# Kernel optimization log

Hardware: AMD Instinct MI355X
Metric: run time of the kernel (lower is better)

## Reference

```python
import jax, jax.numpy as jnp
import numpy as np
import math

B, N, H, C = 1, 2048, 8, 128
PQ, PV, R, CS, CZ = 8, 12, 2, 256, 128
CZ4 = CZ // 4
INF = 1e5
EPS = 1e-8
SOFTPLUS_INV_1 = 0.541324854612918


def _quat_to_rot(q):
    q = q / jnp.linalg.norm(q, axis=-1, keepdims=True)
    w, x, y, z = q[..., 0], q[..., 1], q[..., 2], q[..., 3]
    return jnp.stack([
        jnp.stack([1 - 2 * (y * y + z * z), 2 * (x * y - z * w), 2 * (x * z + y * w)], -1),
        jnp.stack([2 * (x * y + z * w), 1 - 2 * (x * x + z * z), 2 * (y * z - x * w)], -1),
        jnp.stack([2 * (x * z - y * w), 2 * (y * z + x * w), 1 - 2 * (x * x + y * y)], -1),
    ], -2)


def setup_inputs() -> dict:
    key = jax.random.key(0)
    ks = jax.random.split(key, 16)
    rn = lambda k, shape, s=1.0: jax.random.normal(k, shape, dtype=jnp.float32) * s
    hc = H * C
    return dict(
        s=rn(ks[0], (B, N, CS)),
        z_factor_1=rn(ks[1], (B, N, R, CZ)),
        z_factor_2=rn(ks[2], (B, N, R, CZ)),
        rot=_quat_to_rot(rn(ks[3], (B, N, 4))),
        trans=rn(ks[4], (B, N, 3)),
        mask=jnp.ones((B, N), dtype=bool),
        w_q=rn(ks[5], (hc, CS), 0.02), b_q=jnp.zeros((hc,), jnp.float32),
        w_kv=rn(ks[6], (2 * hc, CS), 0.02), b_kv=jnp.zeros((2 * hc,), jnp.float32),
        w_qp=rn(ks[7], (H * PQ * 3, CS), 0.02), b_qp=jnp.zeros((H * PQ * 3,), jnp.float32),
        w_kvp=rn(ks[8], (H * (PQ + PV) * 3, CS), 0.02), b_kvp=jnp.zeros((H * (PQ + PV) * 3,), jnp.float32),
        w_b=rn(ks[9], (H, CZ), 0.02), b_b=jnp.zeros((H,), jnp.float32),
        w_dz=rn(ks[10], (CZ4, CZ), 0.02), b_dz=jnp.zeros((CZ4,), jnp.float32),
        head_weights=jnp.full((H,), SOFTPLUS_INV_1, dtype=jnp.float32),
        w_out=rn(ks[11], (CS, H * (CZ4 + C + 4 * PV)), 0.02), b_out=jnp.zeros((CS,), jnp.float32),
    )


def _lin(x, w, b):
    return x @ w.T + b


def _ipa(s, z1, z2, rot, trans, mask, w_q, b_q, w_kv, b_kv, w_qp, b_qp,
         w_kvp, b_kvp, w_b, b_b, w_dz, b_dz, head_weights, w_out, b_out):
    q = _lin(s, w_q, b_q).reshape(B, N, H, C)
    kv = _lin(s, w_kv, b_kv).reshape(B, N, H, 2 * C)
    k, v = kv[..., :C], kv[..., C:]
    # local points -> global frame: x_glob = R x_loc + t
    qp = _lin(s, w_qp, b_qp).reshape(B, N, H * PQ, 3)
    qp = (jnp.einsum('bnij,bnpj->bnpi', rot, qp) + trans[:, :, None, :]).reshape(B, N, H, PQ, 3)
    kvp = _lin(s, w_kvp, b_kvp).reshape(B, N, H * (PQ + PV), 3)
    kvp = (jnp.einsum('bnij,bnpj->bnpi', rot, kvp) + trans[:, :, None, :]).reshape(B, N, H, PQ + PV, 3)
    kp, vp = kvp[..., :PQ, :], kvp[..., PQ:, :]
    # head weights: softplus init to 1, AF2 scaling sqrt(1/(3*(PQ*9/2)))
    hw = jax.nn.softplus(head_weights) * math.sqrt(1.0 / (3 * (PQ * 9.0 / 2)))
    # low-rank pair bias factors
    b1 = _lin(z1, w_b, b_b)   # [B,N,R,H]
    b2 = _lin(z2, w_b, b_b)
    z1d = _lin(z1, w_dz, b_dz)  # [B,N,R,CZ4]
    z2d = _lin(z2, w_dz, b_dz)
    # logits: scalar QK + point-distance + low-rank pair bias
    scalar = jnp.einsum('bihc,bjhc->bhij', q, k) * math.sqrt(1.0 / (3 * C))
    ptdot = jnp.einsum('bihpx,bjhpx->bhij', qp, kp)
    qn = jnp.sum(qp * qp, axis=(-1, -2))  # [B,N,H]
    kn = jnp.sum(kp * kp, axis=(-1, -2))
    pt_term = hw[None, :, None, None] * (
        ptdot - 0.5 * qn.transpose(0, 2, 1)[:, :, :, None] - 0.5 * kn.transpose(0, 2, 1)[:, :, None, :])
    pair = jnp.einsum('birh,bjrh->bhij', b1, b2)
    mask_bias = jnp.where(mask, 0.0, -INF)[:, None, None, :]
    a = jax.nn.softmax(scalar + pt_term + pair + mask_bias, axis=-1)  # [B,H,N,N]
    # outputs
    o = jnp.einsum('bhij,bjhc->bihc', a, v).reshape(B, N, H * C)
    opt = jnp.einsum('bhij,bjhpx->bihpx', a, vp)  # global-frame points
    opt_loc = jnp.einsum('bnji,bnhpj->bnhpi', rot, opt - trans[:, :, None, None, :])  # R^T (x - t)
    opt_norm = jnp.sqrt(jnp.sum(opt_loc * opt_loc, axis=-1) + EPS)  # [B,N,H,PV]
    oz = jnp.einsum('bhij,bjrc->bihrc', a, z2d)
    opair = jnp.sum(oz * z1d[:, :, None, :, :], axis=3)  # [B,N,H,CZ4]
    feats = jnp.concatenate([
        o,
        opt_loc[..., 0].reshape(B, N, H * PV),
        opt_loc[..., 1].reshape(B, N, H * PV),
        opt_loc[..., 2].reshape(B, N, H * PV),
        opt_norm.reshape(B, N, H * PV),
        opair.reshape(B, N, H * CZ4),
    ], axis=-1)
    return _lin(feats, w_out, b_out)  # [B,N,CS]


def reference(s, z_factor_1, z_factor_2, rot, trans, mask, w_q, b_q, w_kv, b_kv,
              w_qp, b_qp, w_kvp, b_kvp, w_b, b_b, w_dz, b_dz, head_weights,
              w_out, b_out):
    return _ipa(s, z_factor_1, z_factor_2, rot, trans, mask, w_q, b_q, w_kv, b_kv,
                w_qp, b_qp, w_kvp, b_kvp, w_b, b_b, w_dz, b_dz, head_weights,
                w_out, b_out)
```

## Files before the change

kernel.cpp:

```cpp
#include <hip/hip_runtime.h>
#include <math.h>

#define NN   2048
#define HH   8
#define CC   128
#define PQn  8
#define PVn  12
#define RRn  2
#define CSn  256
#define CZn  128
#define CZ4n 32
#define HC   (HH*CC)
#define FEAT (HC + 4*HH*PVn + HH*CZ4n)
#define DA   160
#define DVP  256
#define DVU  240
#define QKV  3840
#define LOG2E 1.4426950408889634f

typedef unsigned short ushort_t;
#define AS1 __attribute__((address_space(1)))
#define AS3 __attribute__((address_space(3)))

using bfrag = __attribute__((ext_vector_type(8))) short;
using ffrag = __attribute__((ext_vector_type(4))) float;

__device__ inline ushort_t f2bf(float x) {
    union { float f; unsigned int u; } v; v.f = x;
    unsigned int r = v.u + 0x7fffu + ((v.u >> 16) & 1u);
    return (ushort_t)(r >> 16);
}
__device__ inline float bf2f(ushort_t x) {
    union { unsigned int u; float f; } v; v.u = ((unsigned int)x) << 16; return v.f;
}

struct CvtArgs {
    const float4* src[12];
    ushort4* dst[12];
    int n4[12];
};
__global__ __launch_bounds__(256) void cvtn_kernel(CvtArgs a)
{
    int i = blockIdx.x * 256 + threadIdx.x;
#pragma unroll
    for (int k = 0; k < 12; ++k) {
        if (i < a.n4[k]) {
            ushort4 o;
            if (a.src[k]) {
                float4 v = a.src[k][i];
                o = make_ushort4(f2bf(v.x), f2bf(v.y), f2bf(v.z), f2bf(v.w));
            } else {
                o = make_ushort4(0, 0, 0, 0);
            }
            a.dst[k][i] = o;
            return;
        }
        i -= a.n4[k];
    }
}

__global__ __launch_bounds__(256) void bgemm_kernel(
    const ushort_t* __restrict__ A, size_t sA,
    const ushort_t* __restrict__ B, size_t sB,
    void* __restrict__ Cv, size_t sC,
    const float* __restrict__ bias, size_t sBias,
    int ldk, int kOff, int kOffPerZ, int kLen, int ldc, int obf)
{
    const int z = blockIdx.z;
    A += (size_t)z * sA;
    B += (size_t)z * sB;
    const float* bp = bias ? (bias + (size_t)z * sBias) : nullptr;
    const int k0beg = kOff + z * kOffPerZ;
    const int r0 = blockIdx.y * 128;
    const int c0 = blockIdx.x * 128;
    __shared__ __align__(16) ushort_t lA[128 * 32];
    __shared__ __align__(16) ushort_t lB[128 * 32];
    const int tid = threadIdx.x;
    const int w = tid >> 6, lane = tid & 63;
    const int wm = (w >> 1) * 64, wn = (w & 1) * 64;
    const int lrA = lane >> 2;
    const int lcA = (lane & 3) * 8;
    ffrag acc[4][4] = {};

    for (int k0 = k0beg; k0 < k0beg + kLen; k0 += 32) {
#pragma unroll
        for (int t = 0; t < 2; ++t) {
            int instr = w * 2 + t;
            int r = instr * 16 + lrA;
            const ushort_t* ga = A + (size_t)(r0 + r) * ldk + k0 + lcA;
            const ushort_t* gb = B + (size_t)(c0 + r) * ldk + k0 + lcA;
            __builtin_amdgcn_global_load_lds((const AS1 void*)ga,
                (AS3 void*)((AS3 ushort_t*)&lA[instr * 512 + lane * 8]), 16, 0, 0);
            __builtin_amdgcn_global_load_lds((const AS1 void*)gb,
                (AS3 void*)((AS3 ushort_t*)&lB[instr * 512 + lane * 8]), 16, 0, 0);
        }
        __syncthreads();
        bfrag af[4], bf[4];
#pragma unroll
        for (int mi = 0; mi < 4; ++mi)
            af[mi] = *(const bfrag*)&lA[(wm + mi * 16 + (lane & 15)) * 32 + (lane >> 4) * 8];
#pragma unroll
        for (int ni = 0; ni < 4; ++ni)
            bf[ni] = *(const bfrag*)&lB[(wn + ni * 16 + (lane & 15)) * 32 + (lane >> 4) * 8];
#pragma unroll
        for (int mi = 0; mi < 4; ++mi)
#pragma unroll
            for (int ni = 0; ni < 4; ++ni)
                acc[mi][ni] = __builtin_amdgcn_mfma_f32_16x16x32_bf16(af[mi], bf[ni], acc[mi][ni], 0, 0, 0);
        __syncthreads();
    }
#pragma unroll
    for (int mi = 0; mi < 4; ++mi) {
#pragma unroll
        for (int ni = 0; ni < 4; ++ni) {
            int col = c0 + wn + ni * 16 + (lane & 15);
            float bv = bp ? bp[col] : 0.f;
#pragma unroll
            for (int rr = 0; rr < 4; ++rr) {
                int row = r0 + wm + mi * 16 + (lane >> 4) * 4 + rr;
                float val = acc[mi][ni][rr] + bv;
                if (obf) ((ushort_t*)Cv)[(size_t)z * sC + (size_t)row * ldc + col] = f2bf(val);
                else     ((float*)Cv)[(size_t)z * sC + (size_t)row * ldc + col] = val;
            }
        }
    }
}

__global__ __launch_bounds__(256) void mgemm_kernel(
    const ushort_t* __restrict__ A0, const ushort_t* __restrict__ B0,
    ushort_t* __restrict__ C0,
    const ushort_t* __restrict__ A1, const ushort_t* __restrict__ B1,
    ushort_t* __restrict__ C1)
{
    const int bx = blockIdx.x;
    const ushort_t *A, *B;
    ushort_t* C;
    int ldk, kLen, ldc, r0, c0;
    if (bx < 480) {
        A = A0; B = B0; C = C0;
        ldk = CSn; kLen = CSn; ldc = QKV;
        r0 = (bx / 30) * 128;
        c0 = (bx % 30) * 128;
    } else {
        int i = bx - 480;
        A = A1; B = B1; C = C1;
        ldk = CZn; kLen = CZn; ldc = 128;
        r0 = i * 128;
        c0 = 0;
    }
    __shared__ __align__(16) ushort_t lA[128 * 32];
    __shared__ __align__(16) ushort_t lB[128 * 32];
    const int tid = threadIdx.x;
    const int w = tid >> 6, lane = tid & 63;
    const int wm = (w >> 1) * 64, wn = (w & 1) * 64;
    const int lrA = lane >> 2;
    const int lcA = (lane & 3) * 8;
    ffrag acc[4][4] = {};

    for (int k0 = 0; k0 < kLen; k0 += 32) {
#pragma unroll
        for (int t = 0; t < 2; ++t) {
            int instr = w * 2 + t;
            int r = instr * 16 + lrA;
            const ushort_t* ga = A + (size_t)(r0 + r) * ldk + k0 + lcA;
            const ushort_t* gb = B + (size_t)(c0 + r) * ldk + k0 + lcA;
            __builtin_amdgcn_global_load_lds((const AS1 void*)ga,
                (AS3 void*)((AS3 ushort_t*)&lA[instr * 512 + lane * 8]), 16, 0, 0);
            __builtin_amdgcn_global_load_lds((const AS1 void*)gb,
                (AS3 void*)((AS3 ushort_t*)&lB[instr * 512 + lane * 8]), 16, 0, 0);
        }
        __syncthreads();
        bfrag af[4], bf[4];
#pragma unroll
        for (int mi = 0; mi < 4; ++mi)
            af[mi] = *(const bfrag*)&lA[(wm + mi * 16 + (lane & 15)) * 32 + (lane >> 4) * 8];
#pragma unroll
        for (int ni = 0; ni < 4; ++ni)
            bf[ni] = *(const bfrag*)&lB[(wn + ni * 16 + (lane & 15)) * 32 + (lane >> 4) * 8];
#pragma unroll
        for (int mi = 0; mi < 4; ++mi)
#pragma unroll
            for (int ni = 0; ni < 4; ++ni)
                acc[mi][ni] = __builtin_amdgcn_mfma_f32_16x16x32_bf16(af[mi], bf[ni], acc[mi][ni], 0, 0, 0);
        __syncthreads();
    }
#pragma unroll
    for (int mi = 0; mi < 4; ++mi) {
#pragma unroll
        for (int ni = 0; ni < 4; ++ni) {
            int col = c0 + wn + ni * 16 + (lane & 15);
#pragma unroll
            for (int rr = 0; rr < 4; ++rr) {
                int row = r0 + wm + mi * 16 + (lane >> 4) * 4 + rr;
                C[(size_t)row * ldc + col] = f2bf(acc[mi][ni][rr]);
            }
        }
    }
}

__global__ __launch_bounds__(256) void prep_kernel(
    const ushort_t* __restrict__ qkv,
    const ushort_t* __restrict__ zproj,
    const float* __restrict__ b_q, const float* __restrict__ b_kv,
    const float* __restrict__ b_qp, const float* __restrict__ b_kvp,
    const float* __restrict__ b_b, const float* __restrict__ b_dz,
    const float* __restrict__ rot, const float* __restrict__ trans,
    const float* __restrict__ hwts,
    ushort_t* __restrict__ qaug, ushort_t* __restrict__ kaug,
    ushort_t* __restrict__ vaug)
{
    const int i = blockIdx.x;
    const int tid = threadIdx.x;
    __shared__ float R[9], t[3];
    __shared__ float qp_l[192], kp_l[192], vp_l[288];
    __shared__ float kn_s[8], hw_s[8];
    __shared__ __align__(16) ushort_t qa_s[8 * DA];
    __shared__ __align__(16) ushort_t ka_s[8 * DA];
    __shared__ __align__(16) ushort_t va_s[8 * DVP];
    if (tid < 9) R[tid] = rot[i*9 + tid];
    if (tid < 3) t[tid] = trans[i*3 + tid];
    if (tid < 8) {
        hw_s[tid] = log1pf(expf(hwts[tid])) * 0.09622504486493763f;
        kn_s[tid] = 0.f;
    }
    __syncthreads();
    if (tid < 64) {
        const ushort_t* v = qkv + (size_t)i*QKV + 3072 + tid*3;
        float vx = bf2f(v[0]) + b_qp[tid*3+0];
        float vy = bf2f(v[1]) + b_qp[tid*3+1];
        float vz = bf2f(v[2]) + b_qp[tid*3+2];
        float X = R[0]*vx + R[1]*vy + R[2]*vz + t[0];
        float Y = R[3]*vx + R[4]*vy + R[5]*vz + t[1];
        float Z = R[6]*vx + R[7]*vy + R[8]*vz + t[2];
        qp_l[tid*3+0] = X; qp_l[tid*3+1] = Y; qp_l[tid*3+2] = Z;
    } else if (tid < 224) {
        int p = tid - 64;
        int h = p / 20, pp = p % 20;
        const ushort_t* v = qkv + (size_t)i*QKV + 3264 + p*3;
        float vx = bf2f(v[0]) + b_kvp[p*3+0];
        float vy = bf2f(v[1]) + b_kvp[p*3+1];
        float vz = bf2f(v[2]) + b_kvp[p*3+2];
        float X = R[0]*vx + R[1]*vy + R[2]*vz + t[0];
        float Y = R[3]*vx + R[4]*vy + R[5]*vz + t[1];
        float Z = R[6]*vx + R[7]*vy + R[8]*vz + t[2];
        if (pp < 8) {
            int b = (h*8 + pp) * 3;
            kp_l[b+0] = X; kp_l[b+1] = Y; kp_l[b+2] = Z;
            atomicAdd(&kn_s[h], X*X + Y*Y + Z*Z);
        } else {
            int b = (h*12 + pp - 8) * 3;
            vp_l[b+0] = X; vp_l[b+1] = Y; vp_l[b+2] = Z;
        }
    }
    __syncthreads();

    const float QS = 0.05103103630798288f * LOG2E;
    for (int idx = tid; idx < 8 * DA; idx += 256) {
        int h = idx / DA, d = idx - h * DA;
        float qv, kv2;
        if (d < 128) {
            qv  = QS * (bf2f(qkv[(size_t)i*QKV + h*128 + d]) + b_q[h*128 + d]);
            kv2 = bf2f(qkv[(size_t)i*QKV + 1024 + h*256 + d]) + b_kv[h*256 + d];
        } else if (d < 152) {
            qv  = hw_s[h] * LOG2E * qp_l[h*24 + d - 128];
            kv2 = kp_l[h*24 + d - 128];
        } else if (d < 154) {
            int r = d - 152;
            qv  = LOG2E * (bf2f(zproj[(size_t)(i*2 + r)*128 + h]) + b_b[h]);
            kv2 = bf2f(zproj[(size_t)(4096 + i*2 + r)*128 + h]) + b_b[h];
        } else if (d == 154) {
            qv  = LOG2E;
            kv2 = -0.5f * hw_s[h] * kn_s[h];
        } else { qv = 0.f; kv2 = 0.f; }
        qa_s[idx] = f2bf(qv);
        ka_s[idx] = f2bf(kv2);
    }
    for (int idx = tid; idx < 8 * DVP; idx += 256) {
        int h = idx >> 8, d = idx & 255;
        float v;
        if (d < 128)       v = bf2f(qkv[(size_t)i*QKV + 1024 + h*256 + 128 + d]) + b_kv[h*256 + 128 + d];
        else if (d < 164)  v = vp_l[h*36 + d - 128];
        else if (d < 196)  v = bf2f(zproj[(size_t)(4096 + i*2 + 0)*128 + 8 + d - 164]) + b_dz[d - 164];
        else if (d < 228)  v = bf2f(zproj[(size_t)(4096 + i*2 + 1)*128 + 8 + d - 196]) + b_dz[d - 196];
        else if (d == 239) v = 1.0f;
        else               v = 0.f;
        va_s[idx] = f2bf(v);
    }
    __syncthreads();

    for (int idx = tid; idx < 576; idx += 256) {
        if (idx < 160) {
            int h = idx / 20, dg = (idx - h*20) * 8;
            *(bfrag*)(qaug + ((size_t)h*NN + i) * DA + dg) = *(const bfrag*)&qa_s[h*DA + dg];
        } else if (idx < 320) {
            int r = idx - 160;
            int h = r / 20, dg = (r - h*20) * 8;
            *(bfrag*)(kaug + ((size_t)h*NN + i) * DA + dg) = *(const bfrag*)&ka_s[h*DA + dg];
        } else {
            int r = idx - 320;
            int h = r >> 5, dg = (r & 31) * 8;
            *(bfrag*)(vaug + ((size_t)h*NN + i) * DVP + dg) = *(const bfrag*)&va_s[h*DVP + dg];
        }
    }
}

__global__ __launch_bounds__(256) void transpose_kernel(
    const ushort_t* __restrict__ in, ushort_t* __restrict__ out)
{
    const int z = blockIdx.z;
    in  += (size_t)z * NN * DVP;
    out += (size_t)z * NN * DVP;
    const int i0 = blockIdx.x * 64;
    const int d0 = blockIdx.y * 64;
    __shared__ __align__(8) ushort_t tb[64][72];
    const int tid = threadIdx.x;
#pragma unroll
    for (int p = 0; p < 4; ++p) {
        int idx = p * 256 + tid;
        int r = idx >> 4, sg = idx & 15;
        ushort4 v = *(const ushort4*)(in + (size_t)(i0 + r) * DVP + d0 + sg * 4);
        *(ushort4*)&tb[r][sg * 4] = v;
    }
    __syncthreads();
#pragma unroll
    for (int p = 0; p < 4; ++p) {
        int idx = p * 256 + tid;
        int d = idx >> 4, ig = idx & 15;
        ushort4 v = make_ushort4(tb[ig*4+0][d], tb[ig*4+1][d],
                                 tb[ig*4+2][d], tb[ig*4+3][d]);
        *(ushort4*)(out + (size_t)(d0 + d) * NN + i0 + ig * 4) = v;
    }
}

__global__ __launch_bounds__(256, 2) void flash_kernel(
    const ushort_t* __restrict__ qaug,
    const ushort_t* __restrict__ kaug,
    const ushort_t* __restrict__ vaugT,
    ushort_t* __restrict__ Opart,
    float* __restrict__ Mpart,
    float* __restrict__ Lpart)
{
    const int i0 = blockIdx.x * 64;
    const int h  = blockIdx.y;
    const int g  = blockIdx.z;

    __shared__ __align__(16) ushort_t Kt[64 * 168];
    __shared__ __align__(16) ushort_t Vt[DVU * 72];
    __shared__ __align__(16) ushort_t Pl[4 * 32 * 40];

    const int tid = threadIdx.x;
    const int w = tid >> 6, lane = tid & 63;
    const int quad = lane >> 4, lc = lane & 15;
    const int rh = w >> 1, jh = w & 1;

    const ushort_t* qh = qaug + (size_t)h * NN * DA;
    const ushort_t* kh = kaug + (size_t)h * NN * DA;
    const ushort_t* vh = vaugT + (size_t)h * DVP * NN;

    bfrag qf[2][5];
#pragma unroll
    for (int mi = 0; mi < 2; ++mi)
#pragma unroll
        for (int ks = 0; ks < 5; ++ks)
            qf[mi][ks] = *(const bfrag*)(qh + (size_t)(i0 + rh*32 + mi*16 + lc) * DA + ks*32 + quad*8);

    ffrag acc[2][15];
#pragma unroll
    for (int mi = 0; mi < 2; ++mi)
#pragma unroll
        for (int dt = 0; dt < 15; ++dt)
            acc[mi][dt] = (ffrag){0.f, 0.f, 0.f, 0.f};
    float m_run = -3.0e38f;

    ushort_t* PlW = Pl + w * (32 * 40);

    for (int it = 0; it < 16; ++it) {
        const int j0 = g * 1024 + it * 64;
#pragma unroll
        for (int k = 0; k < 6; ++k) {
            int idx = k * 256 + tid;
            if (k < 5 || idx < 1344) {
                int row = idx / 21, off = idx - row * 21;
                const ushort_t* src = (off < 20) ? (kh + (size_t)(j0 + row) * DA + off * 8) : kh;
                __builtin_amdgcn_global_load_lds((const AS1 void*)src,
                    (AS3 void*)((AS3 ushort_t*)&Kt[idx * 8]), 16, 0, 0);
            }
        }
#pragma unroll
        for (int k = 0; k < 9; ++k) {
            int idx = k * 256 + tid;
            if (k < 8 || idx < 2160) {
                int row = idx / 9, off = idx - row * 9;
                const ushort_t* src = (off < 8) ? (vh + (size_t)row * NN + j0 + off * 8) : vh;
                __builtin_amdgcn_global_load_lds((const AS1 void*)src,
                    (AS3 void*)((AS3 ushort_t*)&Vt[idx * 8]), 16, 0, 0);
            }
        }
        __syncthreads();

        ffrag sf[2][2];
#pragma unroll
        for (int mi = 0; mi < 2; ++mi)
#pragma unroll
            for (int jt = 0; jt < 2; ++jt)
                sf[mi][jt] = (ffrag){0.f, 0.f, 0.f, 0.f};
#pragma unroll
        for (int ks = 0; ks < 5; ++ks) {
#pragma unroll
            for (int jt = 0; jt < 2; ++jt) {
                bfrag kf = *(const bfrag*)&Kt[(jh*32 + jt*16 + lc) * 168 + ks*32 + quad*8];
#pragma unroll
                for (int mi = 0; mi < 2; ++mi)
                    sf[mi][jt] = __builtin_amdgcn_mfma_f32_16x16x32_bf16(qf[mi][ks], kf, sf[mi][jt], 0, 0, 0);
            }
        }

        float tm = sf[0][0][0];
#pragma unroll
        for (int mi = 0; mi < 2; ++mi)
#pragma unroll
            for (int jt = 0; jt < 2; ++jt)
#pragma unroll
                for (int rr = 0; rr < 4; ++rr)
                    tm = fmaxf(tm, sf[mi][jt][rr]);
#pragma unroll
        for (int d = 1; d < 64; d <<= 1)
            tm = fmaxf(tm, __shfl_xor(tm, d));

        if (tm > m_run) {
            float al = exp2f(m_run - tm);
            m_run = tm;
#pragma unroll
            for (int mi = 0; mi < 2; ++mi)
#pragma unroll
                for (int dt = 0; dt < 15; ++dt)
                    acc[mi][dt] *= al;
        }

#pragma unroll
        for (int mi = 0; mi < 2; ++mi)
#pragma unroll
            for (int rr = 0; rr < 4; ++rr) {
                float p0 = exp2f(sf[mi][0][rr] - m_run);
                float p1 = exp2f(sf[mi][1][rr] - m_run);
                PlW[(mi*16 + quad*4 + rr) * 40 + lc]      = f2bf(p0);
                PlW[(mi*16 + quad*4 + rr) * 40 + 16 + lc] = f2bf(p1);
            }

        bfrag pf0 = *(const bfrag*)&PlW[(0*16 + lc) * 40 + quad*8];
        bfrag pf1 = *(const bfrag*)&PlW[(1*16 + lc) * 40 + quad*8];
#pragma unroll
        for (int dt = 0; dt < 15; ++dt) {
            bfrag vf = *(const bfrag*)&Vt[(dt*16 + lc) * 72 + jh*32 + quad*8];
            acc[0][dt] = __builtin_amdgcn_mfma_f32_16x16x32_bf16(pf0, vf, acc[0][dt], 0, 0, 0);
            acc[1][dt] = __builtin_amdgcn_mfma_f32_16x16x32_bf16(pf1, vf, acc[1][dt], 0, 0, 0);
        }
        __syncthreads();
    }

    const int part = g * 2 + jh;
    ushort_t* Ob = Opart + ((size_t)part * HH + h) * NN * DVU;
#pragma unroll
    for (int mi = 0; mi < 2; ++mi)
#pragma unroll
        for (int dt = 0; dt < 15; ++dt)
#pragma unroll
            for (int rr = 0; rr < 4; ++rr) {
                int row = i0 + rh*32 + mi*16 + quad*4 + rr;
                Ob[(size_t)row * DVU + dt*16 + lc] = f2bf(acc[mi][dt][rr]);
            }
    size_t sb = ((size_t)part * HH + h) * NN;
    if (lane < 32) Mpart[sb + i0 + rh*32 + lane] = m_run;
    if (lc == 15) {
#pragma unroll
        for (int mi = 0; mi < 2; ++mi)
#pragma unroll
            for (int rr = 0; rr < 4; ++rr)
                Lpart[sb + i0 + rh*32 + mi*16 + quad*4 + rr] = acc[mi][14][rr];
    }
}

__global__ __launch_bounds__(256) void combine_kernel(
    const ushort_t* __restrict__ Opart, const float* __restrict__ Mpart,
    const float* __restrict__ Lpart, const ushort_t* __restrict__ zproj,
    const float* __restrict__ b_dz,
    const float* __restrict__ rot, const float* __restrict__ trans,
    ushort_t* __restrict__ feats)
{
    const int i = blockIdx.x;
    const int tid = threadIdx.x;
    __shared__ float wgt[4][8];
    __shared__ float Ol[8][DVU];
    if (tid < 8) {
        int h = tid;
        float mm[4], ll[4];
#pragma unroll
        for (int p = 0; p < 4; ++p) {
            mm[p] = Mpart[((size_t)p * HH + h) * NN + i];
            ll[p] = Lpart[((size_t)p * HH + h) * NN + i];
        }
        float M = fmaxf(fmaxf(mm[0], mm[1]), fmaxf(mm[2], mm[3]));
        float Z = 0.f, e[4];
#pragma unroll
        for (int p = 0; p < 4; ++p) { e[p] = exp2f(mm[p] - M); Z += ll[p] * e[p]; }
        float zi = 1.f / Z;
#pragma unroll
        for (int p = 0; p < 4; ++p) wgt[p][h] = e[p] * zi;
    }
    __syncthreads();
    {
        int h = tid >> 5;
        int dg0 = tid & 31;
        for (int dg = dg0; dg < 60; dg += 32) {
            int d = dg * 4;
            float vx = 0.f, vy = 0.f, vz = 0.f, vw = 0.f;
#pragma unroll
            for (int p = 0; p < 4; ++p) {
                ushort4 u = *(const ushort4*)&Opart[(((size_t)p * HH + h) * NN + i) * DVU + d];
                float wv = wgt[p][h];
                vx += bf2f(u.x) * wv; vy += bf2f(u.y) * wv;
                vz += bf2f(u.z) * wv; vw += bf2f(u.w) * wv;
            }
            Ol[h][d] = vx; Ol[h][d+1] = vy; Ol[h][d+2] = vz; Ol[h][d+3] = vw;
        }
    }
    __syncthreads();

    ushort_t* f = feats + (size_t)i * FEAT;
    {
        int h = tid >> 5;
        int c = (tid * 4) & 127;
        ushort4 o4 = make_ushort4(f2bf(Ol[h][c]), f2bf(Ol[h][c+1]),
                                  f2bf(Ol[h][c+2]), f2bf(Ol[h][c+3]));
        *(ushort4*)(f + tid * 4) = o4;
    }
    if (tid < 96) {
        int h = tid / 12, p = tid % 12;
        const float* Rm = rot + i * 9;
        float ox = Ol[h][128 + p*3 + 0] - trans[i*3 + 0];
        float oy = Ol[h][128 + p*3 + 1] - trans[i*3 + 1];
        float oz = Ol[h][128 + p*3 + 2] - trans[i*3 + 2];
        float lx = Rm[0]*ox + Rm[3]*oy + Rm[6]*oz;
        float ly = Rm[1]*ox + Rm[4]*oy + Rm[7]*oz;
        float lz = Rm[2]*ox + Rm[5]*oy + Rm[8]*oz;
        float nrm = sqrtf(lx*lx + ly*ly + lz*lz + 1e-8f);
        f[1024 + 0*96 + tid] = f2bf(lx);
        f[1024 + 1*96 + tid] = f2bf(ly);
        f[1024 + 2*96 + tid] = f2bf(lz);
        f[1024 + 3*96 + tid] = f2bf(nrm);
    }
    {
        int h = tid >> 5, c = tid & 31;
        float z1d0 = bf2f(zproj[(size_t)(i*2 + 0)*128 + 8 + c]) + b_dz[c];
        float z1d1 = bf2f(zproj[(size_t)(i*2 + 1)*128 + 8 + c]) + b_dz[c];
        f[1408 + tid] = f2bf(Ol[h][164 + c] * z1d0 + Ol[h][196 + c] * z1d1);
    }
}

__global__ __launch_bounds__(256) void wreduce_kernel(
    const float4* __restrict__ part, const float* __restrict__ b_out,
    float4* __restrict__ out)
{
    int i = blockIdx.x * 256 + threadIdx.x;
    const int stride = NN * 256 / 4;
    float4 a = part[i], b = part[i + stride], c = part[i + 2*stride], d = part[i + 3*stride];
    int m = (i & 63) * 4;
    float4 bb = *(const float4*)(b_out + m);
    float4 o;
    o.x = a.x + b.x + c.x + d.x + bb.x;
    o.y = a.y + b.y + c.y + d.y + bb.y;
    o.z = a.z + b.z + c.z + d.z + bb.z;
    o.w = a.w + b.w + c.w + d.w + bb.w;
    out[i] = o;
}

extern "C" void kernel_launch(void* const* d_in, const int* in_sizes, int n_in,
                              void* d_out, int out_size, void* d_ws, size_t ws_size,
                              hipStream_t stream) {
    const float* s     = (const float*)d_in[0];
    const float* z1    = (const float*)d_in[1];
    const float* z2    = (const float*)d_in[2];
    const float* rot   = (const float*)d_in[3];
    const float* trans = (const float*)d_in[4];
    const float* w_q   = (const float*)d_in[6];
    const float* b_q   = (const float*)d_in[7];
    const float* w_kv  = (const float*)d_in[8];
    const float* b_kv  = (const float*)d_in[9];
    const float* w_qp  = (const float*)d_in[10];
    const float* b_qp  = (const float*)d_in[11];
    const float* w_kvp = (const float*)d_in[12];
    const float* b_kvp = (const float*)d_in[13];
    const float* w_b   = (const float*)d_in[14];
    const float* b_b   = (const float*)d_in[15];
    const float* w_dz  = (const float*)d_in[16];
    const float* b_dz  = (const float*)d_in[17];
    const float* hwts  = (const float*)d_in[18];
    const float* w_out = (const float*)d_in[19];
    const float* b_out = (const float*)d_in[20];
    float* out = (float*)d_out;

    char* base = (char*)d_ws;
    const size_t OPART_BYTES = (size_t)4*HH*NN*DVU*2;
    char* S = base;
    ushort_t* s_bf  = (ushort_t*)(S);
    ushort_t* z_bf  = (ushort_t*)(S + 1048576);
    ushort_t* wall  = (ushort_t*)(S + 1048576 + 2097152);
    ushort_t* wz    = (ushort_t*)(S + 1048576 + 2097152 + 1966080);
    ushort_t* qkv   = (ushort_t*)(S + 1048576 + 2097152 + 1966080 + 32768);
    ushort_t* vaug  = (ushort_t*)(S + 1048576 + 2097152 + 1966080 + 32768 + 15728640);
    ushort_t* Opart = (ushort_t*)(S);
    float*    wpart = (float*)(S);
    char* P = base + OPART_BYTES;
    size_t off = 0;
    auto alloc = [&](size_t bytes) -> void* {
        void* p = P + off;
        off += (bytes + 255) & ~(size_t)255;
        return p;
    };
    ushort_t* wout_bf = (ushort_t*)alloc((size_t)CSn*FEAT*2);
    ushort_t* zproj   = (ushort_t*)alloc((size_t)8192*128*2);
    ushort_t* qaug    = (ushort_t*)alloc((size_t)HH*NN*DA*2);
    ushort_t* kaug    = (ushort_t*)alloc((size_t)HH*NN*DA*2);
    ushort_t* vaugT   = (ushort_t*)alloc((size_t)HH*NN*DVP*2);
    float*    Mpart   = (float*)alloc((size_t)4*HH*NN*4);
    float*    Lpart   = (float*)alloc((size_t)4*HH*NN*4);
    ushort_t* feats   = (ushort_t*)alloc((size_t)NN*FEAT*2);

    CvtArgs ca;
    int j = 0; int tot = 0;
    auto job = [&](const float* src, ushort_t* dst, int nElem) {
        ca.src[j] = (const float4*)src; ca.dst[j] = (ushort4*)dst; ca.n4[j] = nElem/4;
        tot += nElem/4; ++j;
    };
    job(s,     s_bf,              NN*CSn);
    job(z1,    z_bf,              4096*128);
    job(z2,    z_bf + 4096*128,   4096*128);
    job(w_q,   wall,              1024*256);
    job(w_kv,  wall + 1024*256,   2048*256);
    job(w_qp,  wall + 3072*256,   192*256);
    job(w_kvp, wall + 3264*256,   480*256);
    job(w_out, wout_bf,           CSn*FEAT);
    job(nullptr, wall + 3744*256, 96*256);
    job(w_b,   wz,                8*128);
    job(w_dz,  wz + 8*128,        32*128);
    job(nullptr, wz + 40*128,     88*128);
    cvtn_kernel<<<(tot + 255)/256, 256, 0, stream>>>(ca);

    mgemm_kernel<<<544, 256, 0, stream>>>(s_bf, wall, qkv, z_bf, wz, zproj);

    prep_kernel<<<NN, 256, 0, stream>>>(qkv, zproj,
                                        b_q, b_kv, b_qp, b_kvp, b_b, b_dz,
                                        rot, trans, hwts, qaug, kaug, vaug);
    transpose_kernel<<<dim3(NN/64, DVP/64, HH), 256, 0, stream>>>(vaug, vaugT);

    flash_kernel<<<dim3(NN/64, HH, 2), 256, 0, stream>>>(
        qaug, kaug, vaugT, Opart, Mpart, Lpart);

    combine_kernel<<<NN, 256, 0, stream>>>(Opart, Mpart, Lpart, zproj, b_dz,
                                           rot, trans, feats);

    bgemm_kernel<<<dim3(CSn/128, NN/128, 4), 256, 0, stream>>>(
        feats, 0, wout_bf, 0, wpart, (size_t)NN*CSn, nullptr, 0,
        FEAT, 0, FEAT/4, FEAT/4, CSn, 0);
    wreduce_kernel<<<NN*CSn/4/256, 256, 0, stream>>>((const float4*)wpart, b_out, (float4*)out);
}
```

Before: 209.1 us.

## Fuse V transpose into prep kernel and replace split-K reduce with atomics

The per-row prep kernel and the separate V transpose kernel are merged into one kernel that works on 64-row tiles per head and writes the transposed V layout directly through shared memory. The split-K output GEMM now atomically adds its partials into the output, which the conversion kernel pre-fills with the bias, so the wreduce kernel and its fp32 partial buffer go away. This cuts two launches and several global round trips. The atomics make the summation order nondeterministic, and the new prep grid has only 256 blocks, which may leave the GPU underfilled.

```diff
diff --git a/kernel.cpp b/kernel.cpp
--- a/kernel.cpp
+++ b/kernel.cpp
@@ -39,9 +39,15 @@
     ushort4* dst[12];
     int n4[12];
 };
-__global__ __launch_bounds__(256) void cvtn_kernel(CvtArgs a)
+__global__ __launch_bounds__(256) void cvtn_kernel(CvtArgs a,
+    float4* __restrict__ outp, const float4* __restrict__ bias4)
 {
     int i = blockIdx.x * 256 + threadIdx.x;
+    if (i < NN * CSn / 4) {
+        outp[i] = bias4[i & 63];
+        return;
+    }
+    i -= NN * CSn / 4;
 #pragma unroll
     for (int k = 0; k < 12; ++k) {
         if (i < a.n4[k]) {
@@ -64,7 +70,7 @@
     const ushort_t* __restrict__ B, size_t sB,
     void* __restrict__ Cv, size_t sC,
     const float* __restrict__ bias, size_t sBias,
-    int ldk, int kOff, int kOffPerZ, int kLen, int ldc, int obf)
+    int ldk, int kOff, int kOffPerZ, int kLen, int ldc, int obf, int atomicOut)
 {
     const int z = blockIdx.z;
     A += (size_t)z * sA;
@@ -119,8 +125,12 @@
             for (int rr = 0; rr < 4; ++rr) {
                 int row = r0 + wm + mi * 16 + (lane >> 4) * 4 + rr;
                 float val = acc[mi][ni][rr] + bv;
-                if (obf) ((ushort_t*)Cv)[(size_t)z * sC + (size_t)row * ldc + col] = f2bf(val);
-                else     ((float*)Cv)[(size_t)z * sC + (size_t)row * ldc + col] = val;
+                if (atomicOut)
+                    unsafeAtomicAdd(&((float*)Cv)[(size_t)z * sC + (size_t)row * ldc + col], val);
+                else if (obf)
+                    ((ushort_t*)Cv)[(size_t)z * sC + (size_t)row * ldc + col] = f2bf(val);
+                else
+                    ((float*)Cv)[(size_t)z * sC + (size_t)row * ldc + col] = val;
             }
         }
     }
@@ -198,7 +208,7 @@
     }
 }
 
-__global__ __launch_bounds__(256) void prep_kernel(
+__global__ __launch_bounds__(256) void prepT_kernel(
     const ushort_t* __restrict__ qkv,
     const ushort_t* __restrict__ zproj,
     const float* __restrict__ b_q, const float* __restrict__ b_kv,
@@ -207,128 +217,115 @@
     const float* __restrict__ rot, const float* __restrict__ trans,
     const float* __restrict__ hwts,
     ushort_t* __restrict__ qaug, ushort_t* __restrict__ kaug,
-    ushort_t* __restrict__ vaug)
+    ushort_t* __restrict__ vaugT)
 {
-    const int i = blockIdx.x;
+    const int i0 = blockIdx.x * 64;
+    const int h  = blockIdx.y;
     const int tid = threadIdx.x;
-    __shared__ float R[9], t[3];
-    __shared__ float qp_l[192], kp_l[192], vp_l[288];
-    __shared__ float kn_s[8], hw_s[8];
-    __shared__ __align__(16) ushort_t qa_s[8 * DA];
-    __shared__ __align__(16) ushort_t ka_s[8 * DA];
-    __shared__ __align__(16) ushort_t va_s[8 * DVP];
-    if (tid < 9) R[tid] = rot[i*9 + tid];
-    if (tid < 3) t[tid] = trans[i*3 + tid];
-    if (tid < 8) {
-        hw_s[tid] = log1pf(expf(hwts[tid])) * 0.09622504486493763f;
-        kn_s[tid] = 0.f;
+    __shared__ float R_s[64][9], t_s[64][3];
+    __shared__ float qp_s[64][8][3], kp_s[64][8][3], vp_s[64][12][3];
+    __shared__ float kn_s[64];
+    __shared__ float hw_sh;
+    __shared__ __align__(16) ushort_t va_s[256][72];
+
+    if (tid == 0) hw_sh = log1pf(expf(hwts[h])) * 0.09622504486493763f;
+    if (tid < 64) kn_s[tid] = 0.f;
+    for (int idx = tid; idx < 64 * 12; idx += 256) {
+        int i = idx / 12, c = idx - i * 12;
+        if (c < 9) R_s[i][c]     = rot[(size_t)(i0 + i) * 9 + c];
+        else       t_s[i][c - 9] = trans[(size_t)(i0 + i) * 3 + (c - 9)];
     }
     __syncthreads();
-    if (tid < 64) {
-        const ushort_t* v = qkv + (size_t)i*QKV + 3072 + tid*3;
-        float vx = bf2f(v[0]) + b_qp[tid*3+0];
-        float vy = bf2f(v[1]) + b_qp[tid*3+1];
-        float vz = bf2f(v[2]) + b_qp[tid*3+2];
-        float X = R[0]*vx + R[1]*vy + R[2]*vz + t[0];
-        float Y = R[3]*vx + R[4]*vy + R[5]*vz + t[1];
-        float Z = R[6]*vx + R[7]*vy + R[8]*vz + t[2];
-        qp_l[tid*3+0] = X; qp_l[tid*3+1] = Y; qp_l[tid*3+2] = Z;
-    } else if (tid < 224) {
-        int p = tid - 64;
-        int h = p / 20, pp = p % 20;
-        const ushort_t* v = qkv + (size_t)i*QKV + 3264 + p*3;
-        float vx = bf2f(v[0]) + b_kvp[p*3+0];
-        float vy = bf2f(v[1]) + b_kvp[p*3+1];
-        float vz = bf2f(v[2]) + b_kvp[p*3+2];
-        float X = R[0]*vx + R[1]*vy + R[2]*vz + t[0];
-        float Y = R[3]*vx + R[4]*vy + R[5]*vz + t[1];
-        float Z = R[6]*vx + R[7]*vy + R[8]*vz + t[2];
-        if (pp < 8) {
-            int b = (h*8 + pp) * 3;
-            kp_l[b+0] = X; kp_l[b+1] = Y; kp_l[b+2] = Z;
-            atomicAdd(&kn_s[h], X*X + Y*Y + Z*Z);
+
+    for (int idx = tid; idx < 64 * 28; idx += 256) {
+        int i = idx / 28, p = idx - i * 28;
+        int gi = i0 + i;
+        const float* R = R_s[i];
+        const float* tt = t_s[i];
+        float vx, vy, vz;
+        if (p < 8) {
+            int gp = (h * 8 + p) * 3;
+            const ushort_t* v = qkv + (size_t)gi * QKV + 3072 + gp;
+            vx = bf2f(v[0]) + b_qp[gp + 0];
+            vy = bf2f(v[1]) + b_qp[gp + 1];
+            vz = bf2f(v[2]) + b_qp[gp + 2];
+            float X = R[0]*vx + R[1]*vy + R[2]*vz + tt[0];
+            float Y = R[3]*vx + R[4]*vy + R[5]*vz + tt[1];
+            float Z = R[6]*vx + R[7]*vy + R[8]*vz + tt[2];
+            qp_s[i][p][0] = X; qp_s[i][p][1] = Y; qp_s[i][p][2] = Z;
         } else {
-            int b = (h*12 + pp - 8) * 3;
-            vp_l[b+0] = X; vp_l[b+1] = Y; vp_l[b+2] = Z;
+            int pp = p - 8;
+            int gp = (h * 20 + pp) * 3;
+            const ushort_t* v = qkv + (size_t)gi * QKV + 3264 + gp;
+            vx = bf2f(v[0]) + b_kvp[gp + 0];
+            vy = bf2f(v[1]) + b_kvp[gp + 1];
+            vz = bf2f(v[2]) + b_kvp[gp + 2];
+            float X = R[0]*vx + R[1]*vy + R[2]*vz + tt[0];
+            float Y = R[3]*vx + R[4]*vy + R[5]*vz + tt[1];
+            float Z = R[6]*vx + R[7]*vy + R[8]*vz + tt[2];
+            if (pp < 8) {
+                kp_s[i][pp][0] = X; kp_s[i][pp][1] = Y; kp_s[i][pp][2] = Z;
+                atomicAdd(&kn_s[i], X*X + Y*Y + Z*Z);
+            } else {
+                vp_s[i][pp-8][0] = X; vp_s[i][pp-8][1] = Y; vp_s[i][pp-8][2] = Z;
+            }
         }
     }
     __syncthreads();
 
+    const float hw = hw_sh;
     const float QS = 0.05103103630798288f * LOG2E;
-    for (int idx = tid; idx < 8 * DA; idx += 256) {
-        int h = idx / DA, d = idx - h * DA;
-        float qv, kv2;
-        if (d < 128) {
-            qv  = QS * (bf2f(qkv[(size_t)i*QKV + h*128 + d]) + b_q[h*128 + d]);
-            kv2 = bf2f(qkv[(size_t)i*QKV + 1024 + h*256 + d]) + b_kv[h*256 + d];
-        } else if (d < 152) {
-            qv  = hw_s[h] * LOG2E * qp_l[h*24 + d - 128];
-            kv2 = kp_l[h*24 + d - 128];
-        } else if (d < 154) {
-            int r = d - 152;
-            qv  = LOG2E * (bf2f(zproj[(size_t)(i*2 + r)*128 + h]) + b_b[h]);
-            kv2 = bf2f(zproj[(size_t)(4096 + i*2 + r)*128 + h]) + b_b[h];
-        } else if (d == 154) {
-            qv  = LOG2E;
-            kv2 = -0.5f * hw_s[h] * kn_s[h];
-        } else { qv = 0.f; kv2 = 0.f; }
-        qa_s[idx] = f2bf(qv);
-        ka_s[idx] = f2bf(kv2);
-    }
-    for (int idx = tid; idx < 8 * DVP; idx += 256) {
-        int h = idx >> 8, d = idx & 255;
-        float v;
-        if (d < 128)       v = bf2f(qkv[(size_t)i*QKV + 1024 + h*256 + 128 + d]) + b_kv[h*256 + 128 + d];
-        else if (d < 164)  v = vp_l[h*36 + d - 128];
-        else if (d < 196)  v = bf2f(zproj[(size_t)(4096 + i*2 + 0)*128 + 8 + d - 164]) + b_dz[d - 164];
-        else if (d < 228)  v = bf2f(zproj[(size_t)(4096 + i*2 + 1)*128 + 8 + d - 196]) + b_dz[d - 196];
-        else if (d == 239) v = 1.0f;
-        else               v = 0.f;
-        va_s[idx] = f2bf(v);
+    for (int idx = tid; idx < 64 * 40; idx += 256) {
+        int i = idx / 40, g = idx - i * 40, d0 = g * 4;
+        int gi = i0 + i;
+        ushort_t q4[4], k4[4];
+#pragma unroll
+        for (int j = 0; j < 4; ++j) {
+            int d = d0 + j;
+            float qv, kv2;
+            if (d < 128) {
+                qv  = QS * (bf2f(qkv[(size_t)gi*QKV + h*128 + d]) + b_q[h*128 + d]);
+                kv2 = bf2f(qkv[(size_t)gi*QKV + 1024 + h*256 + d]) + b_kv[h*256 + d];
+            } else if (d < 152) {
+                int dd = d - 128, pt = dd / 3, x = dd - pt * 3;
+                qv  = hw * LOG2E * qp_s[i][pt][x];
+                kv2 = kp_s[i][pt][x];
+            } else if (d < 154) {
+                int r = d - 152;
+                qv  = LOG2E * (bf2f(zproj[(size_t)(gi*2 + r)*128 + h]) + b_b[h]);
+                kv2 = bf2f(zproj[(size_t)(4096 + gi*2 + r)*128 + h]) + b_b[h];
+            } else if (d == 154) {
+                qv  = LOG2E;
+                kv2 = -0.5f * hw * kn_s[i];
+            } else { qv = 0.f; kv2 = 0.f; }
+            q4[j] = f2bf(qv); k4[j] = f2bf(kv2);
+        }
+        *(ushort4*)(qaug + ((size_t)h*NN + gi)*DA + d0) = make_ushort4(q4[0], q4[1], q4[2], q4[3]);
+        *(ushort4*)(kaug + ((size_t)h*NN + gi)*DA + d0) = make_ushort4(k4[0], k4[1], k4[2], k4[3]);
+    }
+
+    for (int idx = tid; idx < 64 * 64; idx += 256) {
+        int i = idx & 63, dg = idx >> 6, d0 = dg * 4;
+        int gi = i0 + i;
+#pragma unroll
+        for (int j = 0; j < 4; ++j) {
+            int d = d0 + j;
+            float v;
+            if (d < 128)       v = bf2f(qkv[(size_t)gi*QKV + 1024 + h*256 + 128 + d]) + b_kv[h*256 + 128 + d];
+            else if (d < 164)  { int dd = d - 128, pt = dd / 3, x = dd - pt*3; v = vp_s[i][pt][x]; }
+            else if (d < 196)  v = bf2f(zproj[(size_t)(4096 + gi*2 + 0)*128 + 8 + d - 164]) + b_dz[d - 164];
+            else if (d < 228)  v = bf2f(zproj[(size_t)(4096 + gi*2 + 1)*128 + 8 + d - 196]) + b_dz[d - 196];
+            else if (d == 239) v = 1.0f;
+            else               v = 0.f;
+            va_s[d][i] = f2bf(v);
+        }
     }
     __syncthreads();
 
-    for (int idx = tid; idx < 576; idx += 256) {
-        if (idx < 160) {
-            int h = idx / 20, dg = (idx - h*20) * 8;
-            *(bfrag*)(qaug + ((size_t)h*NN + i) * DA + dg) = *(const bfrag*)&qa_s[h*DA + dg];
-        } else if (idx < 320) {
-            int r = idx - 160;
-            int h = r / 20, dg = (r - h*20) * 8;
-            *(bfrag*)(kaug + ((size_t)h*NN + i) * DA + dg) = *(const bfrag*)&ka_s[h*DA + dg];
-        } else {
-            int r = idx - 320;
-            int h = r >> 5, dg = (r & 31) * 8;
-            *(bfrag*)(vaug + ((size_t)h*NN + i) * DVP + dg) = *(const bfrag*)&va_s[h*DVP + dg];
-        }
-    }
-}
-
-__global__ __launch_bounds__(256) void transpose_kernel(
-    const ushort_t* __restrict__ in, ushort_t* __restrict__ out)
-{
-    const int z = blockIdx.z;
-    in  += (size_t)z * NN * DVP;
-    out += (size_t)z * NN * DVP;
-    const int i0 = blockIdx.x * 64;
-    const int d0 = blockIdx.y * 64;
-    __shared__ __align__(8) ushort_t tb[64][72];
-    const int tid = threadIdx.x;
-#pragma unroll
-    for (int p = 0; p < 4; ++p) {
-        int idx = p * 256 + tid;
-        int r = idx >> 4, sg = idx & 15;
-        ushort4 v = *(const ushort4*)(in + (size_t)(i0 + r) * DVP + d0 + sg * 4);
-        *(ushort4*)&tb[r][sg * 4] = v;
-    }
-    __syncthreads();
-#pragma unroll
-    for (int p = 0; p < 4; ++p) {
-        int idx = p * 256 + tid;
-        int d = idx >> 4, ig = idx & 15;
-        ushort4 v = make_ushort4(tb[ig*4+0][d], tb[ig*4+1][d],
-                                 tb[ig*4+2][d], tb[ig*4+3][d]);
-        *(ushort4*)(out + (size_t)(d0 + d) * NN + i0 + ig * 4) = v;
+    for (int idx = tid; idx < 256 * 16; idx += 256) {
+        int d = idx >> 4, g = idx & 15;
+        ushort4 v = *(const ushort4*)&va_s[d][g * 4];
+        *(ushort4*)(vaugT + ((size_t)h*DVP + d)*NN + i0 + g*4) = v;
     }
 }
 
@@ -555,23 +552,6 @@
         float z1d1 = bf2f(zproj[(size_t)(i*2 + 1)*128 + 8 + c]) + b_dz[c];
         f[1408 + tid] = f2bf(Ol[h][164 + c] * z1d0 + Ol[h][196 + c] * z1d1);
     }
-}
-
-__global__ __launch_bounds__(256) void wreduce_kernel(
-    const float4* __restrict__ part, const float* __restrict__ b_out,
-    float4* __restrict__ out)
-{
-    int i = blockIdx.x * 256 + threadIdx.x;
-    const int stride = NN * 256 / 4;
-    float4 a = part[i], b = part[i + stride], c = part[i + 2*stride], d = part[i + 3*stride];
-    int m = (i & 63) * 4;
-    float4 bb = *(const float4*)(b_out + m);
-    float4 o;
-    o.x = a.x + b.x + c.x + d.x + bb.x;
-    o.y = a.y + b.y + c.y + d.y + bb.y;
-    o.z = a.z + b.z + c.z + d.z + bb.z;
-    o.w = a.w + b.w + c.w + d.w + bb.w;
-    out[i] = o;
 }
 
 extern "C" void kernel_launch(void* const* d_in, const int* in_sizes, int n_in,
@@ -607,9 +587,7 @@
     ushort_t* wall  = (ushort_t*)(S + 1048576 + 2097152);
     ushort_t* wz    = (ushort_t*)(S + 1048576 + 2097152 + 1966080);
     ushort_t* qkv   = (ushort_t*)(S + 1048576 + 2097152 + 1966080 + 32768);
-    ushort_t* vaug  = (ushort_t*)(S + 1048576 + 2097152 + 1966080 + 32768 + 15728640);
     ushort_t* Opart = (ushort_t*)(S);
-    float*    wpart = (float*)(S);
     char* P = base + OPART_BYTES;
     size_t off = 0;
     auto alloc = [&](size_t bytes) -> void* {
@@ -644,14 +622,14 @@
     job(w_b,   wz,                8*128);
     job(w_dz,  wz + 8*128,        32*128);
     job(nullptr, wz + 40*128,     88*128);
-    cvtn_kernel<<<(tot + 255)/256, 256, 0, stream>>>(ca);
+    tot += NN*CSn/4;
+    cvtn_kernel<<<(tot + 255)/256, 256, 0, stream>>>(ca, (float4*)out, (const float4*)b_out);
 
     mgemm_kernel<<<544, 256, 0, stream>>>(s_bf, wall, qkv, z_bf, wz, zproj);
 
-    prep_kernel<<<NN, 256, 0, stream>>>(qkv, zproj,
-                                        b_q, b_kv, b_qp, b_kvp, b_b, b_dz,
-                                        rot, trans, hwts, qaug, kaug, vaug);
-    transpose_kernel<<<dim3(NN/64, DVP/64, HH), 256, 0, stream>>>(vaug, vaugT);
+    prepT_kernel<<<dim3(32, 8), 256, 0, stream>>>(
+        qkv, zproj, b_q, b_kv, b_qp, b_kvp, b_b, b_dz,
+        rot, trans, hwts, qaug, kaug, vaugT);
 
     flash_kernel<<<dim3(NN/64, HH, 2), 256, 0, stream>>>(
         qaug, kaug, vaugT, Opart, Mpart, Lpart);
@@ -660,7 +638,6 @@
                                            rot, trans, feats);
 
     bgemm_kernel<<<dim3(CSn/128, NN/128, 4), 256, 0, stream>>>(
-        feats, 0, wout_bf, 0, wpart, (size_t)NN*CSn, nullptr, 0,
-        FEAT, 0, FEAT/4, FEAT/4, CSn, 0);
-    wreduce_kernel<<<NN*CSn/4/256, 256, 0, stream>>>((const float4*)wpart, b_out, (float4*)out);
-}
+        feats, 0, wout_bf, 0, out, 0, nullptr, 0,
+        FEAT, 0, FEAT/4, FEAT/4, CSn, 0, 1);
+}
```

Result: slower. 227.6 us (+8.8%).
